# Optimization experiments

Hardware: AMD Instinct MI355X
Metric: run time of the kernel (lower is better)

Reference implementation:

```python
import jax, jax.numpy as jnp
from jax import lax
import numpy as np

B, N = 512, 256
INF = jnp.float32(1e30)


def setup_inputs() -> dict:
    key = jax.random.key(0)
    k1, k2 = jax.random.split(key)
    costs = jax.random.normal(k1, (B, N, N), dtype=jnp.float32)
    pad_mask = jax.random.randint(k2, (B, N), 0, 2).astype(bool)
    return {"costs": costs, "pad_mask": pad_mask}


def _solve_lap(cost):
    """Jonker-Volgenant shortest-augmenting-path LAP, same math as
    scipy.optimize.linear_sum_assignment. cost: [n, n], rows=objects,
    cols=predictions. Returns col4row[n]: assigned column per row."""
    n = cost.shape[0]
    idx = jnp.arange(n, dtype=jnp.int32)

    def assign_row(cur_row, state):
        u, v, col4row, row4col = state
        cur_row = jnp.int32(cur_row)

        def path_cond(c):
            return c[2] < 0

        def path_body(c):
            i, minval, sink, shortest, pathrow, SR, SC = c
            SR = SR.at[i].set(True)
            r = minval + cost[i] - u[i] - v  # reduced cost of extending path via row i
            upd = jnp.logical_and(~SC, r < shortest)
            shortest = jnp.where(upd, r, shortest)
            pathrow = jnp.where(upd, i, pathrow)
            masked = jnp.where(SC, INF, shortest)
            j = jnp.argmin(masked).astype(jnp.int32)
            minval = masked[j]
            SC = SC.at[j].set(True)
            nxt = row4col[j]
            sink = jnp.where(nxt < 0, j, jnp.int32(-1))
            i = jnp.where(nxt < 0, i, nxt)
            return (i, minval, sink, shortest, pathrow, SR, SC)

        init = (cur_row, jnp.float32(0.0), jnp.int32(-1),
                jnp.full((n,), INF, jnp.float32),
                jnp.full((n,), -1, jnp.int32),
                jnp.zeros((n,), bool), jnp.zeros((n,), bool))
        i, minval, sink, shortest, pathrow, SR, SC = lax.while_loop(
            path_cond, path_body, init)

        # dual updates (Crouse 2016 / scipy lsap)
        u = u.at[cur_row].add(minval)
        others = jnp.logical_and(SR, idx != cur_row)
        u = u + jnp.where(others, minval - shortest[jnp.clip(col4row, 0, n - 1)], 0.0)
        v = v - jnp.where(SC, minval - shortest, 0.0)

        # augment along the alternating path back to cur_row
        def aug_cond(c):
            return ~c[3]

        def aug_body(c):
            j, col4row, row4col, done = c
            i = pathrow[j]
            row4col = row4col.at[j].set(i)
            j_next = col4row[i]
            col4row = col4row.at[i].set(j)
            return (j_next, col4row, row4col, i == cur_row)

        _, col4row, row4col, _ = lax.while_loop(
            aug_cond, aug_body, (sink, col4row, row4col, jnp.bool_(False)))
        return (u, v, col4row, row4col)

    state = (jnp.zeros((n,), jnp.float32), jnp.zeros((n,), jnp.float32),
             jnp.full((n,), -1, jnp.int32), jnp.full((n,), -1, jnp.int32))
    _, _, col4row, _ = lax.fori_loop(0, n, assign_row, state)
    return col4row


def _match_one(cost_t, n_k):
    # cost_t: [n_obj_slots, n_pred] (== costs[k].T); n_k: number of valid objects
    n = cost_t.shape[0]
    idx = jnp.arange(n, dtype=jnp.int32)
    rows_valid = idx < n_k
    # padded object rows get constant cost -> assignment of real rows unchanged
    P = jnp.where(rows_valid[:, None], cost_t, 0.0)
    cols = _solve_lap(P)
    # prediction indices used by real objects (cols is a permutation)
    used = jnp.zeros((n,), bool).at[cols].set(rows_valid)
    # unused prediction indices, ascending, placed first
    order = jnp.argsort(jnp.where(used, idx + n, idx)).astype(jnp.int32)
    fill = order[jnp.clip(idx - n_k, 0, n - 1)]
    return jnp.where(rows_valid, cols, fill)


def _forward(costs, pad_mask):
    costs = jnp.nan_to_num(costs.astype(jnp.float32),
                           nan=1e6, posinf=1e6, neginf=1e6)
    n_k = jnp.sum(pad_mask, axis=1).astype(jnp.int32)  # valid objects per batch
    cost_t = jnp.swapaxes(costs, 1, 2)                 # [B, n_obj, n_pred]
    return jax.vmap(_match_one)(cost_t, n_k)


def reference(costs, pad_mask):
    return _forward(costs, pad_mask)
```

## Files before the change

kernel.cpp:

```cpp
#include <hip/hip_runtime.h>
#include <math.h>

#define NB 512
#define NN 256
#define NCACHE 61
#define LAP_INF 1e30f

#define WS_NK_OFF 1024
#define WS_RMV_OFF 8192
#define WS_RMA_OFF (8192 + 512 * 1024)
#define WS_PT_OFF_FULL (8192 + 1024 * 1024)
#define WS_PT_OFF_R4 8192

__global__ __launch_bounds__(1024)
void detect_kernel(const unsigned int* __restrict__ pw, int* __restrict__ flag) {
  __shared__ int notInt, notFloat;
  if (threadIdx.x == 0) { notInt = 0; notFloat = 0; }
  __syncthreads();
  int li = 0, lf = 0;
  for (int t = threadIdx.x; t < 32768; t += 1024) {
    unsigned int w = pw[t];
    if (w > 1u) li = 1;
    if (w != 0u && w != 0x3F800000u) lf = 1;
  }
  if (li) atomicOr(&notInt, 1);
  if (lf) atomicOr(&notFloat, 1);
  __syncthreads();
  if (threadIdx.x == 0) flag[0] = (!notInt) ? 1 : ((!notFloat) ? 2 : 0);
}

__global__ __launch_bounds__(64)
void nk_kernel(const void* __restrict__ pm, const int* __restrict__ flag,
               int* __restrict__ nk) {
  const int k = blockIdx.x;
  const int lane = threadIdx.x;
  const int fl = flag[0];
  int cnt4 = 0;
  if (fl == 1) {
    const int* p = ((const int*)pm) + k * NN;
#pragma unroll
    for (int q = 0; q < 4; ++q) cnt4 += (p[lane * 4 + q] != 0);
  } else if (fl == 2) {
    const float* p = ((const float*)pm) + k * NN;
#pragma unroll
    for (int q = 0; q < 4; ++q) cnt4 += (p[lane * 4 + q] != 0.0f);
  } else {
    const unsigned char* p = ((const unsigned char*)pm) + k * NN;
#pragma unroll
    for (int q = 0; q < 4; ++q) cnt4 += (p[lane * 4 + q] != 0);
  }
#pragma unroll
  for (int off = 32; off > 0; off >>= 1) cnt4 += __shfl_down(cnt4, off);
  if (lane == 0) nk[k] = cnt4;
}

__global__ __launch_bounds__(256)
void transpose_kernel(const float* __restrict__ in, float* __restrict__ out,
                      const int* __restrict__ nk) {
  const int k = blockIdx.z;
  const int i0 = blockIdx.x * 32;
  int bnd = nk[k];
  bnd = bnd > NCACHE ? bnd : NCACHE;
  if (i0 >= bnd) return;
  __shared__ float tile[32][33];
  const float* A = in + ((size_t)k << 16);
  float* Bp = out + ((size_t)k << 16);
  const int tx = threadIdx.x, ty = threadIdx.y;
  const int j0 = blockIdx.y * 32;
#pragma unroll
  for (int r = 0; r < 32; r += 8) {
    float x = A[(size_t)(j0 + ty + r) * NN + (i0 + tx)];
    tile[ty + r][tx] = isfinite(x) ? x : 1e6f;
  }
  __syncthreads();
#pragma unroll
  for (int r = 0; r < 32; r += 8) {
    Bp[(size_t)(i0 + ty + r) * NN + (j0 + tx)] = tile[tx][ty + r];
  }
}

template <int CTRL>
__device__ __forceinline__ unsigned dpp_min_step(unsigned x) {
  unsigned y = (unsigned)__builtin_amdgcn_update_dpp((int)x, (int)x, CTRL, 0xF, 0xF, false);
  return y < x ? y : x;
}
__device__ __forceinline__ unsigned wave_min_u32(unsigned x) {
  x = dpp_min_step<0xB1>(x);
  x = dpp_min_step<0x4E>(x);
  x = dpp_min_step<0x141>(x);
  x = dpp_min_step<0x140>(x);
  x = dpp_min_step<0x142>(x);
  x = dpp_min_step<0x143>(x);
  return (unsigned)__builtin_amdgcn_readlane((int)x, 63);
}
__device__ __forceinline__ unsigned f2o(float f) {
  unsigned x = __float_as_uint(f);
  return x ^ ((unsigned)((int)x >> 31) | 0x80000000u);
}
__device__ __forceinline__ float o2f(unsigned m) {
  unsigned x = (m & 0x80000000u) ? (m & 0x7FFFFFFFu) : ~m;
  return __uint_as_float(x);
}
__device__ __forceinline__ int sel4(const int a[4], int s) {
  return (s == 0) ? a[0] : (s == 1) ? a[1] : (s == 2) ? a[2] : a[3];
}
__device__ __forceinline__ void set4(int a[4], int s, int v) {
  if (s == 0) a[0] = v; else if (s == 1) a[1] = v;
  else if (s == 2) a[2] = v; else a[3] = v;
}
__device__ __forceinline__ void setf4(float a[4], int s, float v) {
  if (s == 0) a[0] = v; else if (s == 1) a[1] = v;
  else if (s == 2) a[2] = v; else a[3] = v;
}

__global__ __launch_bounds__(256)
void rowmin_kernel(const float* __restrict__ Pt, const int* __restrict__ nk,
                   float* __restrict__ rmv, int* __restrict__ rma) {
  const int k = blockIdx.x;
  const int wid = threadIdx.x >> 6, lane = threadIdx.x & 63;
  const int row = blockIdx.y * 4 + wid;
  int bnd = nk[k];
  bnd = bnd > NCACHE ? bnd : NCACHE;
  if (row >= bnd) return;
  const float4 rv = *(const float4*)(Pt + ((size_t)k << 16) + (size_t)row * NN + lane * 4);
  float bv = rv.x; int bj = lane * 4;
  if (rv.y < bv) { bv = rv.y; bj = lane * 4 + 1; }
  if (rv.z < bv) { bv = rv.z; bj = lane * 4 + 2; }
  if (rv.w < bv) { bv = rv.w; bj = lane * 4 + 3; }
  const unsigned m = f2o(bv);
  const unsigned g = wave_min_u32(m);
  const unsigned long long cm = __ballot(m == g);
  const int owner = __ffsll(cm) - 1;
  const int ja = __builtin_amdgcn_readlane(bj, owner);
  if (lane == 0) {
    rmv[k * NN + row] = o2f(g);
    rma[k * NN + row] = ja;
  }
}

__global__ __launch_bounds__(64)
void lap_kernel(const float* __restrict__ costs, const void* __restrict__ pm,
                const int* __restrict__ flag, const int* __restrict__ nkArr,
                const float* __restrict__ rmv, const int* __restrict__ rma,
                const float* __restrict__ Pt, int* __restrict__ out, int mode) {
  const int k = blockIdx.x;
  const int lane = threadIdx.x;

  __shared__ __align__(16) float rowCache[NCACHE][NN];
  __shared__ int freeRowsL[NN];
  __shared__ int winnerL[NN];

  const float* PtK = Pt + ((size_t)k << 16);
  const float* costK = costs + ((size_t)k << 16);

  int n_k;
  if (mode >= 1) {
    n_k = nkArr[k];
  } else {
    const int fl = flag[0];
    int cnt4 = 0;
    if (fl == 1) {
      const int* p = ((const int*)pm) + k * NN;
#pragma unroll
      for (int q = 0; q < 4; ++q) cnt4 += (p[lane * 4 + q] != 0);
    } else if (fl == 2) {
      const float* p = ((const float*)pm) + k * NN;
#pragma unroll
      for (int q = 0; q < 4; ++q) cnt4 += (p[lane * 4 + q] != 0.0f);
    } else {
      const unsigned char* p = ((const unsigned char*)pm) + k * NN;
#pragma unroll
      for (int q = 0; q < 4; ++q) cnt4 += (p[lane * 4 + q] != 0);
    }
#pragma unroll
    for (int off = 32; off > 0; off >>= 1) cnt4 += __shfl_down(cnt4, off);
    n_k = __shfl(cnt4, 0);
  }

  float vv[4] = {0.f, 0.f, 0.f, 0.f};
  float uu[4] = {0.f, 0.f, 0.f, 0.f};
  int r4c[4] = {-1, -1, -1, -1};
  int c4r[4] = {-1, -1, -1, -1};
  int ja[4] = {-1, -1, -1, -1};
  int nfree = 0;

  if (mode == 2) {
#pragma unroll 1
    for (int base = 0; base + 8 <= NCACHE; base += 8) {
      float4 b[8];
#pragma unroll
      for (int r = 0; r < 8; ++r)
        b[r] = *(const float4*)(PtK + (size_t)(base + r) * NN + lane * 4);
#pragma unroll
      for (int r = 0; r < 8; ++r)
        *(float4*)(&rowCache[base + r][lane * 4]) = b[r];
    }
    {
      const int base = (NCACHE / 8) * 8;
      float4 b[NCACHE - (NCACHE / 8) * 8];
#pragma unroll
      for (int r = 0; r < NCACHE - (NCACHE / 8) * 8; ++r)
        b[r] = *(const float4*)(PtK + (size_t)(base + r) * NN + lane * 4);
#pragma unroll
      for (int r = 0; r < NCACHE - (NCACHE / 8) * 8; ++r)
        *(float4*)(&rowCache[base + r][lane * 4]) = b[r];
    }

    const float4 mv = *(const float4*)(rmv + k * NN + lane * 4);
    const int4 av = *(const int4*)(rma + k * NN + lane * 4);
    uu[0] = mv.x; uu[1] = mv.y; uu[2] = mv.z; uu[3] = mv.w;
    ja[0] = av.x; ja[1] = av.y; ja[2] = av.z; ja[3] = av.w;
#pragma unroll
    for (int q = 0; q < 4; ++q)
      if (lane * 4 + q >= n_k) uu[q] = 0.f;

    for (int t = lane; t < NN; t += 64) winnerL[t] = 0x7FFFFFFF;
    __syncthreads();
#pragma unroll
    for (int q = 0; q < 4; ++q) {
      const int row = lane * 4 + q;
      if (row < n_k) atomicMin(&winnerL[ja[q]], row);
    }
    __syncthreads();
#pragma unroll
    for (int s = 0; s < 4; ++s) {
      const int w = winnerL[lane * 4 + s];
      r4c[s] = (w == 0x7FFFFFFF) ? -1 : w;
    }
    unsigned fm = 0;
#pragma unroll
    for (int q = 0; q < 4; ++q) {
      const int row = lane * 4 + q;
      const bool valid = row < n_k;
      const bool won = valid && (winnerL[ja[q]] == row);
      c4r[q] = won ? ja[q] : -1;
      if (valid && !won) fm |= (1u << q);
    }
    const int cnt = __popc(fm);
    int x = cnt;
#pragma unroll
    for (int off = 1; off < 64; off <<= 1) {
      const int y = __shfl_up(x, off);
      if (lane >= off) x += y;
    }
    nfree = __shfl(x, 63);
    int pos = x - cnt;
#pragma unroll
    for (int q = 0; q < 4; ++q) {
      if ((fm >> q) & 1u) { freeRowsL[pos] = lane * 4 + q; ++pos; }
    }
    __syncthreads();
  } else {
    if (mode >= 1) {
      const float4* s4 = (const float4*)PtK;
      float4* c4 = (float4*)rowCache;
      for (int t = lane; t < NCACHE * (NN / 4); t += 64) c4[t] = s4[t];
    } else {
      for (int e = lane; e < NCACHE * NN; e += 64) {
        const int i = e >> 8, j = e & 255;
        float x = costK[(size_t)j * NN + i];
        rowCache[i][j] = isfinite(x) ? x : 1e6f;
      }
    }
    __syncthreads();
    float4 carry = {0.f, 0.f, 0.f, 0.f};
    for (int r = 0; r < n_k; ++r) {
      float cc[4];
      if (r < NCACHE) {
        const float4 rv = *(const float4*)(&rowCache[r][lane * 4]);
        cc[0] = rv.x; cc[1] = rv.y; cc[2] = rv.z; cc[3] = rv.w;
      } else if (mode >= 1) {
        cc[0] = carry.x; cc[1] = carry.y; cc[2] = carry.z; cc[3] = carry.w;
      } else {
#pragma unroll
        for (int q = 0; q < 4; ++q) {
          float x = costK[(size_t)(lane * 4 + q) * NN + r];
          cc[q] = isfinite(x) ? x : 1e6f;
        }
      }
      if (mode >= 1 && r + 1 >= NCACHE && r + 1 < n_k)
        carry = *(const float4*)(PtK + (size_t)(r + 1) * NN + lane * 4);

      unsigned lbv = 0xFFFFFFFFu;
      int lbq = 0;
#pragma unroll
      for (int q = 0; q < 4; ++q) {
        const unsigned m = f2o(cc[q]);
        if (m < lbv) { lbv = m; lbq = q; }
      }
      const unsigned gv = wave_min_u32(lbv);
      const unsigned long long cmask = __ballot(lbv == gv);
      const int owner = __ffsll((unsigned long long)cmask) - 1;
      const int js = (owner << 2) + __builtin_amdgcn_readlane(lbq, owner);
      if (lane == (r >> 2)) setf4(uu, r & 3, o2f(gv));
      const int occ = __builtin_amdgcn_readlane(sel4(r4c, js & 3), owner);
      if (occ < 0) {
        if (lane == owner) set4(r4c, js & 3, r);
        if (lane == (r >> 2)) set4(c4r, r & 3, js);
      } else {
        if (lane == 0) freeRowsL[nfree] = r;
        nfree++;
      }
    }
    __syncthreads();
  }

  for (int t = 0; t < nfree; ++t) {
    const int cur = freeRowsL[t];
    float sh[4] = {LAP_INF, LAP_INF, LAP_INF, LAP_INF};
    int pr[4] = {-1, -1, -1, -1};
    unsigned scm = 0;
    unsigned srm = 0;
    float minval = 0.f;
    int i = cur, sink = -1;

    while (sink < 0) {
      const int islot = i & 3, iowner = i >> 2;
      if (lane == iowner) srm |= (1u << islot);
      const float su = (islot == 0) ? uu[0] : (islot == 1) ? uu[1]
                     : (islot == 2) ? uu[2] : uu[3];
      const float ui = __int_as_float(
          __builtin_amdgcn_readlane(__float_as_int(su), iowner));

      float cc[4];
      if (i < NCACHE) {
        const float4 rv = *(const float4*)(&rowCache[i][lane * 4]);
        cc[0] = rv.x; cc[1] = rv.y; cc[2] = rv.z; cc[3] = rv.w;
      } else if (mode >= 1) {
        const float4 rv = *(const float4*)(PtK + (size_t)i * NN + lane * 4);
        cc[0] = rv.x; cc[1] = rv.y; cc[2] = rv.z; cc[3] = rv.w;
      } else {
#pragma unroll
        for (int q = 0; q < 4; ++q) {
          float x = costK[(size_t)(lane * 4 + q) * NN + i];
          cc[q] = isfinite(x) ? x : 1e6f;
        }
      }

      unsigned mq[4];
#pragma unroll
      for (int q = 0; q < 4; ++q) {
        float r = minval + cc[q];
        r = r - ui;
        r = r - vv[q];
        const bool sc = (scm >> q) & 1u;
        if (!sc && r < sh[q]) { sh[q] = r; pr[q] = i; }
        mq[q] = sc ? 0xFFFFFFFFu : f2o(sh[q]);
      }
      unsigned ma = mq[0]; int qa = 0;
      if (mq[1] < ma) { ma = mq[1]; qa = 1; }
      unsigned mc = mq[2]; int qc = 2;
      if (mq[3] < mc) { mc = mq[3]; qc = 3; }
      unsigned lbv = ma; int lbq = qa;
      if (mc < ma) { lbv = mc; lbq = qc; }

      const int cand = sel4(r4c, lbq);
      const unsigned pack = (unsigned)lbq | ((unsigned)(cand + 1) << 2);

      const unsigned gv = wave_min_u32(lbv);
      minval = o2f(gv);
      const unsigned long long cmask = __ballot(lbv == gv);
      const int owner = __ffsll((unsigned long long)cmask) - 1;
      const unsigned pk = (unsigned)__builtin_amdgcn_readlane((int)pack, owner);
      const int js = (owner << 2) + (int)(pk & 3u);
      if (lane == owner) scm |= (1u << lbq);
      const int nxt = (int)(pk >> 2) - 1;
      if (nxt < 0) sink = js; else i = nxt;
    }

    float gv4[4];
#pragma unroll
    for (int q = 0; q < 4; ++q) {
      const int tgt = c4r[q] >= 0 ? c4r[q] : 0;
      const int srcLane = tgt >> 2, slot = tgt & 3;
      const float g0 = __shfl(sh[0], srcLane);
      const float g1 = __shfl(sh[1], srcLane);
      const float g2 = __shfl(sh[2], srcLane);
      const float g3 = __shfl(sh[3], srcLane);
      gv4[q] = (slot == 0) ? g0 : (slot == 1) ? g1 : (slot == 2) ? g2 : g3;
    }
#pragma unroll
    for (int q = 0; q < 4; ++q) {
      if ((srm >> q) & 1u) {
        const int row = lane * 4 + q;
        if (row == cur) uu[q] = uu[q] + minval;
        else uu[q] = uu[q] + (minval - gv4[q]);
      }
      if ((scm >> q) & 1u) vv[q] = vv[q] - (minval - sh[q]);
    }

    int j = sink;
    bool done = false;
    while (!done) {
      const int pi = __builtin_amdgcn_readlane(sel4(pr, j & 3), j >> 2);
      if (lane == (j >> 2)) set4(r4c, j & 3, pi);
      const int jn = __builtin_amdgcn_readlane(sel4(c4r, pi & 3), pi >> 2);
      if (lane == (pi >> 2)) set4(c4r, pi & 3, j);
      done = (pi == cur);
      j = jn;
    }
  }

  int* outK = out + k * NN;
#pragma unroll
  for (int q = 0; q < 4; ++q) {
    const int row = lane * 4 + q;
    if (row < n_k) outK[row] = c4r[q];
  }
  unsigned um = 0;
#pragma unroll
  for (int s = 0; s < 4; ++s)
    if (r4c[s] < 0) um |= (1u << s);
  const int uc = __popc(um);
  int ux = uc;
#pragma unroll
  for (int off = 1; off < 64; off <<= 1) {
    const int uy = __shfl_up(ux, off);
    if (lane >= off) ux += uy;
  }
  int upos = ux - uc;
#pragma unroll
  for (int s = 0; s < 4; ++s) {
    if ((um >> s) & 1u) { outK[n_k + upos] = lane * 4 + s; ++upos; }
  }
}

extern "C" void kernel_launch(void* const* d_in, const int* in_sizes, int n_in,
                              void* d_out, int out_size, void* d_ws, size_t ws_size,
                              hipStream_t stream) {
  const float* costs = (const float*)d_in[0];
  const void* pm = d_in[1];
  int* out = (int*)d_out;

  int* flag = (int*)d_ws;
  int* nk = (int*)((char*)d_ws + WS_NK_OFF);
  const size_t ptBytes = (size_t)NB * NN * NN * sizeof(float);

  int mode;
  float* rmv; int* rma; float* Pt;
  if (ws_size >= WS_PT_OFF_FULL + ptBytes) {
    mode = 2;
    rmv = (float*)((char*)d_ws + WS_RMV_OFF);
    rma = (int*)((char*)d_ws + WS_RMA_OFF);
    Pt = (float*)((char*)d_ws + WS_PT_OFF_FULL);
  } else if (ws_size >= WS_PT_OFF_R4 + ptBytes) {
    mode = 1;
    rmv = (float*)d_ws; rma = (int*)d_ws;
    Pt = (float*)((char*)d_ws + WS_PT_OFF_R4);
  } else {
    mode = 0;
    rmv = (float*)d_ws; rma = (int*)d_ws;
    Pt = (float*)costs;
  }

  detect_kernel<<<1, 1024, 0, stream>>>((const unsigned int*)pm, flag);
  nk_kernel<<<NB, 64, 0, stream>>>(pm, flag, nk);
  if (mode >= 1) {
    dim3 g(8, 8, NB), b(32, 8);
    transpose_kernel<<<g, b, 0, stream>>>(costs, Pt, nk);
  }
  if (mode == 2) {
    dim3 g(NB, 64);
    rowmin_kernel<<<g, 256, 0, stream>>>(Pt, nk, rmv, rma);
  }
  lap_kernel<<<NB, 64, 0, stream>>>(costs, pm, flag, nk, rmv, rma, Pt, out, mode);
}
```

Baseline: 357.1 us.

## Fuse transpose and per-row minimum into one kernel with packed keys

Merges the transpose kernel and the separate rowmin kernel into one kernel. Each block now walks all column tiles for its 32 rows and tracks the running minimum as a packed 64-bit (ordered value, column) key. This removes one launch and the re-read of the transposed matrix. In exchange the grid drops from 8x8xNB to 8x1xNB blocks, each doing serial loop work, which reduces parallelism in that stage.

```diff
diff --git a/kernel.cpp b/kernel.cpp
--- a/kernel.cpp
+++ b/kernel.cpp
@@ -7,8 +7,7 @@
 #define LAP_INF 1e30f
 
 #define WS_NK_OFF 1024
-#define WS_RMV_OFF 8192
-#define WS_RMA_OFF (8192 + 512 * 1024)
+#define WS_RMK_OFF 8192
 #define WS_PT_OFF_FULL (8192 + 1024 * 1024)
 #define WS_PT_OFF_R4 8192
 
@@ -52,6 +51,62 @@
 #pragma unroll
   for (int off = 32; off > 0; off >>= 1) cnt4 += __shfl_down(cnt4, off);
   if (lane == 0) nk[k] = cnt4;
+}
+
+__device__ __forceinline__ unsigned f2o(float f) {
+  unsigned x = __float_as_uint(f);
+  return x ^ ((unsigned)((int)x >> 31) | 0x80000000u);
+}
+__device__ __forceinline__ float o2f(unsigned m) {
+  unsigned x = (m & 0x80000000u) ? (m & 0x7FFFFFFFu) : ~m;
+  return __uint_as_float(x);
+}
+
+__global__ __launch_bounds__(256)
+void transpose_rowmin_kernel(const float* __restrict__ in,
+                             float* __restrict__ out,
+                             const int* __restrict__ nk,
+                             unsigned long long* __restrict__ rmk) {
+  const int k = blockIdx.z;
+  const int i0 = blockIdx.x * 32;
+  int bnd = nk[k];
+  bnd = bnd > NCACHE ? bnd : NCACHE;
+  if (i0 >= bnd) return;
+  __shared__ float tile[32][33];
+  __shared__ unsigned long long keyL[8][32];
+  const float* A = in + ((size_t)k << 16);
+  float* Bp = out + ((size_t)k << 16);
+  const int tx = threadIdx.x, ty = threadIdx.y;
+  unsigned long long best = ~0ull;
+#pragma unroll 1
+  for (int j0 = 0; j0 < NN; j0 += 32) {
+#pragma unroll
+    for (int r = 0; r < 32; r += 8) {
+      float x = A[(size_t)(j0 + ty + r) * NN + (i0 + tx)];
+      tile[ty + r][tx] = isfinite(x) ? x : 1e6f;
+    }
+    __syncthreads();
+#pragma unroll
+    for (int r = 0; r < 32; r += 8) {
+      Bp[(size_t)(i0 + ty + r) * NN + (j0 + tx)] = tile[tx][ty + r];
+      const float v = tile[ty + r][tx];
+      const unsigned long long key =
+          ((unsigned long long)f2o(v) << 32) | (unsigned)(j0 + ty + r);
+      if (key < best) best = key;
+    }
+    __syncthreads();
+  }
+  keyL[ty][tx] = best;
+  __syncthreads();
+  if (ty == 0) {
+    unsigned long long b = keyL[0][tx];
+#pragma unroll
+    for (int s = 1; s < 8; ++s) {
+      const unsigned long long c = keyL[s][tx];
+      if (c < b) b = c;
+    }
+    rmk[k * NN + i0 + tx] = b;
+  }
 }
 
 __global__ __launch_bounds__(256)
@@ -93,14 +148,6 @@
   x = dpp_min_step<0x143>(x);
   return (unsigned)__builtin_amdgcn_readlane((int)x, 63);
 }
-__device__ __forceinline__ unsigned f2o(float f) {
-  unsigned x = __float_as_uint(f);
-  return x ^ ((unsigned)((int)x >> 31) | 0x80000000u);
-}
-__device__ __forceinline__ float o2f(unsigned m) {
-  unsigned x = (m & 0x80000000u) ? (m & 0x7FFFFFFFu) : ~m;
-  return __uint_as_float(x);
-}
 __device__ __forceinline__ int sel4(const int a[4], int s) {
   return (s == 0) ? a[0] : (s == 1) ? a[1] : (s == 2) ? a[2] : a[3];
 }
@@ -113,35 +160,10 @@
   else if (s == 2) a[2] = v; else a[3] = v;
 }
 
-__global__ __launch_bounds__(256)
-void rowmin_kernel(const float* __restrict__ Pt, const int* __restrict__ nk,
-                   float* __restrict__ rmv, int* __restrict__ rma) {
-  const int k = blockIdx.x;
-  const int wid = threadIdx.x >> 6, lane = threadIdx.x & 63;
-  const int row = blockIdx.y * 4 + wid;
-  int bnd = nk[k];
-  bnd = bnd > NCACHE ? bnd : NCACHE;
-  if (row >= bnd) return;
-  const float4 rv = *(const float4*)(Pt + ((size_t)k << 16) + (size_t)row * NN + lane * 4);
-  float bv = rv.x; int bj = lane * 4;
-  if (rv.y < bv) { bv = rv.y; bj = lane * 4 + 1; }
-  if (rv.z < bv) { bv = rv.z; bj = lane * 4 + 2; }
-  if (rv.w < bv) { bv = rv.w; bj = lane * 4 + 3; }
-  const unsigned m = f2o(bv);
-  const unsigned g = wave_min_u32(m);
-  const unsigned long long cm = __ballot(m == g);
-  const int owner = __ffsll(cm) - 1;
-  const int ja = __builtin_amdgcn_readlane(bj, owner);
-  if (lane == 0) {
-    rmv[k * NN + row] = o2f(g);
-    rma[k * NN + row] = ja;
-  }
-}
-
 __global__ __launch_bounds__(64)
 void lap_kernel(const float* __restrict__ costs, const void* __restrict__ pm,
                 const int* __restrict__ flag, const int* __restrict__ nkArr,
-                const float* __restrict__ rmv, const int* __restrict__ rma,
+                const unsigned long long* __restrict__ rmk,
                 const float* __restrict__ Pt, int* __restrict__ out, int mode) {
   const int k = blockIdx.x;
   const int lane = threadIdx.x;
@@ -206,13 +228,16 @@
         *(float4*)(&rowCache[base + r][lane * 4]) = b[r];
     }
 
-    const float4 mv = *(const float4*)(rmv + k * NN + lane * 4);
-    const int4 av = *(const int4*)(rma + k * NN + lane * 4);
-    uu[0] = mv.x; uu[1] = mv.y; uu[2] = mv.z; uu[3] = mv.w;
-    ja[0] = av.x; ja[1] = av.y; ja[2] = av.z; ja[3] = av.w;
-#pragma unroll
-    for (int q = 0; q < 4; ++q)
+    const unsigned long long* rk = rmk + k * NN + lane * 4;
+    unsigned long long kk[4];
+#pragma unroll
+    for (int q = 0; q < 4; ++q) kk[q] = rk[q];
+#pragma unroll
+    for (int q = 0; q < 4; ++q) {
+      uu[q] = o2f((unsigned)(kk[q] >> 32));
+      ja[q] = (int)(unsigned)(kk[q] & 0xFFFFFFFFu);
       if (lane * 4 + q >= n_k) uu[q] = 0.f;
+    }
 
     for (int t = lane; t < NN; t += 64) winnerL[t] = 0x7FFFFFFF;
     __syncthreads();
@@ -437,31 +462,29 @@
   const size_t ptBytes = (size_t)NB * NN * NN * sizeof(float);
 
   int mode;
-  float* rmv; int* rma; float* Pt;
+  unsigned long long* rmk; float* Pt;
   if (ws_size >= WS_PT_OFF_FULL + ptBytes) {
     mode = 2;
-    rmv = (float*)((char*)d_ws + WS_RMV_OFF);
-    rma = (int*)((char*)d_ws + WS_RMA_OFF);
+    rmk = (unsigned long long*)((char*)d_ws + WS_RMK_OFF);
     Pt = (float*)((char*)d_ws + WS_PT_OFF_FULL);
   } else if (ws_size >= WS_PT_OFF_R4 + ptBytes) {
     mode = 1;
-    rmv = (float*)d_ws; rma = (int*)d_ws;
+    rmk = (unsigned long long*)d_ws;
     Pt = (float*)((char*)d_ws + WS_PT_OFF_R4);
   } else {
     mode = 0;
-    rmv = (float*)d_ws; rma = (int*)d_ws;
+    rmk = (unsigned long long*)d_ws;
     Pt = (float*)costs;
   }
 
   detect_kernel<<<1, 1024, 0, stream>>>((const unsigned int*)pm, flag);
   nk_kernel<<<NB, 64, 0, stream>>>(pm, flag, nk);
-  if (mode >= 1) {
+  if (mode == 2) {
+    dim3 g(8, 1, NB), b(32, 8);
+    transpose_rowmin_kernel<<<g, b, 0, stream>>>(costs, Pt, nk, rmk);
+  } else if (mode == 1) {
     dim3 g(8, 8, NB), b(32, 8);
     transpose_kernel<<<g, b, 0, stream>>>(costs, Pt, nk);
   }
-  if (mode == 2) {
-    dim3 g(NB, 64);
-    rowmin_kernel<<<g, 256, 0, stream>>>(Pt, nk, rmv, rma);
-  }
-  lap_kernel<<<NB, 64, 0, stream>>>(costs, pm, flag, nk, rmv, rma, Pt, out, mode);
-}
+  lap_kernel<<<NB, 64, 0, stream>>>(costs, pm, flag, nk, rmk, Pt, out, mode);
+}
```

After: 348.0 us. -2.5%, faster.
